# Performance work log

Hardware: AMD Instinct MI355X
Metric: run time of the kernel (lower is better)

## Reference

```python
import jax, jax.numpy as jnp
import numpy as np
import math

IN_FEATURES = 1024
OUT_FEATURES = 1024
N_BANK = 8192
N_LAYER = 12
N_EMBD = 1024


def setup_inputs() -> dict:
    key = jax.random.key(0)
    kq, kk, kv = jax.random.split(key, 3)
    q = jax.random.normal(kq, (4, 2048, IN_FEATURES), dtype=jnp.float32)
    k = 0.02 * jax.random.normal(kk, (N_BANK, IN_FEATURES), dtype=jnp.float32)
    v_std = 2.0 / N_LAYER / math.sqrt(N_EMBD)
    v = v_std * jax.random.normal(kv, (N_BANK, OUT_FEATURES), dtype=jnp.float32)
    return {"q": q, "k": k, "v": v}


def reference(q, k, v):
    # scores: [B, T, N]
    scores = jnp.einsum("btd,nd->btn", q, k)
    # row-wise L2 normalization, scaled by sqrt(N), then exact (erf) GELU
    sqrt_n = jnp.sqrt(jnp.asarray(scores.shape[-1], scores.dtype))
    norm = jnp.linalg.norm(scores, axis=-1, keepdims=True)
    gated = jax.nn.gelu(scores / norm * sqrt_n, approximate=False)
    # out: [B, T, out_features]
    return jnp.einsum("btn,no->bto", gated, v)
```

## Files before the change

kernel.cpp:

```cpp
#include <hip/hip_runtime.h>
#include <hip/hip_bf16.h>
#include <math.h>


#define MROWS 8192
#define DIN   1024
#define NBANK 8192
#define DOUT  1024

typedef float  f32x4  __attribute__((ext_vector_type(4)));
typedef __bf16 bf16x8 __attribute__((ext_vector_type(8)));

__device__ __forceinline__ float bf2f(unsigned short u) {
  union { unsigned int i; float f; } x; x.i = ((unsigned int)u) << 16; return x.f;
}
__device__ __forceinline__ unsigned short f2bf(float f) {
  union { float f; unsigned int i; } x; x.f = f;
  unsigned int u = x.i;
  unsigned int r = (u + 0x7fffu + ((u >> 16) & 1u)) >> 16;
  return (unsigned short)r;
}

__global__ void cvt_kernel(const float* __restrict__ src,
                           unsigned short* __restrict__ dst, int n) {
  int i = (blockIdx.x * 256 + threadIdx.x) * 4;
  if (i >= n) return;
  float4 vv = *(const float4*)(src + i);
  ushort4 o;
  o.x = f2bf(vv.x); o.y = f2bf(vv.y); o.z = f2bf(vv.z); o.w = f2bf(vv.w);
  *(ushort4*)(dst + i) = o;
}

__global__ void transpose_cvt_kernel(const float* __restrict__ src,
                                     unsigned short* __restrict__ dst,
                                     int R, int C) {
  __shared__ float tile[32][33];
  int c0 = blockIdx.x * 32, r0 = blockIdx.y * 32;
  for (int i = threadIdx.y; i < 32; i += 8)
    tile[i][threadIdx.x] = src[(size_t)(r0 + i) * C + c0 + threadIdx.x];
  __syncthreads();
  for (int i = threadIdx.y; i < 32; i += 8)
    dst[(size_t)(c0 + i) * R + r0 + threadIdx.x] = f2bf(tile[threadIdx.x][i]);
}

__global__ void zero_f32_kernel(float* __restrict__ p, int n4) {
  int i = blockIdx.x * 256 + threadIdx.x;
  if (i < n4) ((float4*)p)[i] = make_float4(0.f, 0.f, 0.f, 0.f);
}

__global__ __launch_bounds__(256, 2) void gemm1_kernel(
    const unsigned short* __restrict__ A, const unsigned short* __restrict__ B,
    unsigned short* __restrict__ C, float* __restrict__ sumsq) {
  __shared__ unsigned short As[128 * 64];
  __shared__ unsigned short Bs[128 * 64];
  const int K = DIN, ldc = NBANK;

  const int tid  = threadIdx.x;
  const int lane = tid & 63;
  const int wave = tid >> 6;
  const int wm   = (wave >> 1) * 64;
  const int wn   = (wave & 1) * 64;
  const int quad = lane >> 4;
  const int l16  = lane & 15;

  const size_t m0 = (size_t)blockIdx.y * 128;
  const size_t n0 = (size_t)blockIdx.x * 128;

  const int srow = tid >> 3;
  const int scol = (tid & 7) * 8;
  const unsigned short* Ag = A + (m0 + srow) * (size_t)K + scol;
  const unsigned short* Bg = B + (n0 + srow) * (size_t)K + scol;
  unsigned short* AsW = As + tid * 8;
  unsigned short* BsW = Bs + tid * 8;

  const unsigned short* ArP = As + (wm + l16) * 64 + quad * 8;
  const unsigned short* BrP = Bs + (wn + l16) * 64 + quad * 8;

  f32x4 acc[4][4];
#pragma unroll
  for (int i = 0; i < 4; i++)
#pragma unroll
    for (int j = 0; j < 4; j++) {
      f32x4 z = {0.f, 0.f, 0.f, 0.f};
      acc[i][j] = z;
    }

  for (int k0 = 0; k0 < K; k0 += 64) {
#pragma unroll
    for (int i = 0; i < 4; i++) {
      __builtin_amdgcn_global_load_lds(
          (const __attribute__((address_space(1))) unsigned int*)(Ag + (size_t)i * 32 * K + k0),
          (__attribute__((address_space(3))) unsigned int*)(AsW + i * 2048), 16, 0, 0);
      __builtin_amdgcn_global_load_lds(
          (const __attribute__((address_space(1))) unsigned int*)(Bg + (size_t)i * 32 * K + k0),
          (__attribute__((address_space(3))) unsigned int*)(BsW + i * 2048), 16, 0, 0);
    }
    __syncthreads();

#pragma unroll
    for (int kk = 0; kk < 2; kk++) {
      bf16x8 af[4], bfr[4];
#pragma unroll
      for (int i = 0; i < 4; i++) af[i] = *(const bf16x8*)(ArP + i * 16 * 64 + kk * 32);
#pragma unroll
      for (int j = 0; j < 4; j++) bfr[j] = *(const bf16x8*)(BrP + j * 16 * 64 + kk * 32);
#pragma unroll
      for (int i = 0; i < 4; i++)
#pragma unroll
        for (int j = 0; j < 4; j++)
          acc[i][j] = __builtin_amdgcn_mfma_f32_16x16x32_bf16(af[i], bfr[j],
                                                              acc[i][j], 0, 0, 0);
    }
    __syncthreads();
  }

#pragma unroll
  for (int i = 0; i < 4; i++)
#pragma unroll
    for (int r = 0; r < 4; r++) {
      size_t row = m0 + wm + i * 16 + quad * 4 + r;
      float s = 0.f;
#pragma unroll
      for (int j = 0; j < 4; j++) {
        float val = acc[i][j][r];
        s += val * val;
        C[row * (size_t)ldc + n0 + wn + j * 16 + l16] = f2bf(val);
      }
      s += __shfl_xor(s, 1);
      s += __shfl_xor(s, 2);
      s += __shfl_xor(s, 4);
      s += __shfl_xor(s, 8);
      if (l16 == 0) atomicAdd(&sumsq[row], s);
    }
}

__global__ void finalize_scale_kernel(float* __restrict__ s) {
  int i = blockIdx.x * 256 + threadIdx.x;
  if (i < MROWS) s[i] = sqrtf((float)NBANK / s[i]);
}

__global__ void gelu_kernel(unsigned short* __restrict__ S,
                            const float* __restrict__ scale) {
  size_t idx = ((size_t)blockIdx.x * 256 + threadIdx.x) * 8;
  int row = (int)(idx >> 13);
  float sc = scale[row];
  uint4 vv = *(const uint4*)(S + idx);
  unsigned int w[4] = {vv.x, vv.y, vv.z, vv.w};
#pragma unroll
  for (int e = 0; e < 4; e++) {
    float x0 = bf2f((unsigned short)(w[e] & 0xffffu)) * sc;
    float x1 = bf2f((unsigned short)(w[e] >> 16)) * sc;
    float g0 = 0.5f * x0 * (1.0f + erff(x0 * 0.70710678118654752f));
    float g1 = 0.5f * x1 * (1.0f + erff(x1 * 0.70710678118654752f));
    w[e] = (unsigned int)f2bf(g0) | ((unsigned int)f2bf(g1) << 16);
  }
  uint4 o; o.x = w[0]; o.y = w[1]; o.z = w[2]; o.w = w[3];
  *(uint4*)(S + idx) = o;
}

__global__ __launch_bounds__(512, 2) void gemm2_kernel(
    const unsigned short* __restrict__ A,
    const unsigned short* __restrict__ B,
    float* __restrict__ C) {
  __shared__ unsigned short As[128 * 64];
  __shared__ unsigned short Bs[256 * 64];
  const int K = NBANK, ldc = DOUT;

  const int tid  = threadIdx.x;
  const int lane = tid & 63;
  const int wave = tid >> 6;
  const int wm   = (wave >> 2) * 64;
  const int wn   = (wave & 3) * 64;
  const int quad = lane >> 4;
  const int l16  = lane & 15;

  const size_t m0 = (size_t)blockIdx.y * 128;
  const size_t n0 = (size_t)blockIdx.x * 256;
  const int    ks = blockIdx.z * (K / 2);

  const int srow = tid >> 3;
  const int scol = (tid & 7) * 8;
  const unsigned short* Ag = A + (m0 + srow) * (size_t)K + scol + ks;
  const unsigned short* Bg = B + (n0 + srow) * (size_t)K + scol + ks;
  unsigned short* AsW = As + tid * 8;
  unsigned short* BsW = Bs + tid * 8;

  const unsigned short* ArP = As + (wm + l16) * 64 + quad * 8;
  const unsigned short* BrP = Bs + (wn + l16) * 64 + quad * 8;

  f32x4 acc[4][4];
#pragma unroll
  for (int i = 0; i < 4; i++)
#pragma unroll
    for (int j = 0; j < 4; j++) {
      f32x4 z = {0.f, 0.f, 0.f, 0.f};
      acc[i][j] = z;
    }

  for (int k0 = 0; k0 < K / 2; k0 += 64) {
#pragma unroll
    for (int i = 0; i < 2; i++)
      __builtin_amdgcn_global_load_lds(
          (const __attribute__((address_space(1))) unsigned int*)(Ag + (size_t)i * 64 * K + k0),
          (__attribute__((address_space(3))) unsigned int*)(AsW + i * 4096), 16, 0, 0);
#pragma unroll
    for (int i = 0; i < 4; i++)
      __builtin_amdgcn_global_load_lds(
          (const __attribute__((address_space(1))) unsigned int*)(Bg + (size_t)i * 64 * K + k0),
          (__attribute__((address_space(3))) unsigned int*)(BsW + i * 4096), 16, 0, 0);
    __syncthreads();

#pragma unroll
    for (int kk = 0; kk < 2; kk++) {
      bf16x8 af[4], bfr[4];
#pragma unroll
      for (int i = 0; i < 4; i++) af[i] = *(const bf16x8*)(ArP + i * 16 * 64 + kk * 32);
#pragma unroll
      for (int j = 0; j < 4; j++) bfr[j] = *(const bf16x8*)(BrP + j * 16 * 64 + kk * 32);
#pragma unroll
      for (int i = 0; i < 4; i++)
#pragma unroll
        for (int j = 0; j < 4; j++)
          acc[i][j] = __builtin_amdgcn_mfma_f32_16x16x32_bf16(af[i], bfr[j],
                                                              acc[i][j], 0, 0, 0);
    }
    __syncthreads();
  }

#pragma unroll
  for (int i = 0; i < 4; i++)
#pragma unroll
    for (int j = 0; j < 4; j++)
#pragma unroll
      for (int r = 0; r < 4; r++) {
        size_t row = m0 + wm + i * 16 + quad * 4 + r;
        size_t col = n0 + wn + j * 16 + l16;
        atomicAdd(&C[row * (size_t)ldc + col], acc[i][j][r]);
      }
}

extern "C" void kernel_launch(void* const* d_in, const int* in_sizes, int n_in,
                              void* d_out, int out_size, void* d_ws, size_t ws_size,
                              hipStream_t stream) {
  const float* q = (const float*)d_in[0];
  const float* k = (const float*)d_in[1];
  const float* v = (const float*)d_in[2];
  float* out = (float*)d_out;

  char* ws = (char*)d_ws;
  const size_t MB = 1024ull * 1024ull;
  unsigned short* qb     = (unsigned short*)(ws);
  unsigned short* kb     = (unsigned short*)(ws + 16 * MB);
  unsigned short* vbT    = (unsigned short*)(ws + 32 * MB);
  unsigned short* scores = (unsigned short*)(ws + 48 * MB);
  float*          scale  = (float*)(ws + 176 * MB);

  const int nqk = MROWS * DIN;

  zero_f32_kernel<<<(MROWS * DOUT / 4 + 255) / 256, 256, 0, stream>>>(out,
                                                                      MROWS * DOUT / 4);
  zero_f32_kernel<<<(MROWS / 4 + 255) / 256, 256, 0, stream>>>(scale, MROWS / 4);

  cvt_kernel<<<nqk / 1024, 256, 0, stream>>>(q, qb, nqk);
  cvt_kernel<<<nqk / 1024, 256, 0, stream>>>(k, kb, nqk);
  transpose_cvt_kernel<<<dim3(DOUT / 32, NBANK / 32), dim3(32, 8), 0, stream>>>(
      v, vbT, NBANK, DOUT);

  gemm1_kernel<<<dim3(NBANK / 128, MROWS / 128), 256, 0, stream>>>(qb, kb, scores,
                                                                   scale);

  finalize_scale_kernel<<<MROWS / 256, 256, 0, stream>>>(scale);

  gelu_kernel<<<(MROWS * (size_t)NBANK) / (256 * 8), 256, 0, stream>>>(scores, scale);

  gemm2_kernel<<<dim3(DOUT / 256, MROWS / 128, 2), 512, 0, stream>>>(scores, vbT, out);
}
```

Before: 581.1 us.

## Fuse GELU into second GEMM A-tile load and add register-prefetch swizzled LDS

The standalone GELU pass over the 8192x8192 bf16 score matrix is removed. Instead, gemm2 applies the scale and erf-GELU to each A tile in registers before storing it to LDS. Both GEMMs switch from direct global-to-LDS loads to register prefetch of the next tile, overlapped with MFMA work, and use an XOR-swizzled LDS layout to avoid bank conflicts. gemm2 also shrinks from a 128x256 tile with 512 threads to 128x128 with 256 threads. GELU is now recomputed by every column block of gemm2 (8x redundant), which trades the saved memory round trip for extra ALU work and register pressure.

```diff
diff --git a/kernel.cpp b/kernel.cpp
--- a/kernel.cpp
+++ b/kernel.cpp
@@ -67,14 +67,22 @@
   const size_t n0 = (size_t)blockIdx.x * 128;
 
   const int srow = tid >> 3;
-  const int scol = (tid & 7) * 8;
-  const unsigned short* Ag = A + (m0 + srow) * (size_t)K + scol;
-  const unsigned short* Bg = B + (n0 + srow) * (size_t)K + scol;
-  unsigned short* AsW = As + tid * 8;
-  unsigned short* BsW = Bs + tid * 8;
-
-  const unsigned short* ArP = As + (wm + l16) * 64 + quad * 8;
-  const unsigned short* BrP = Bs + (wn + l16) * 64 + quad * 8;
+  const int sc8  = tid & 7;
+  const unsigned short* Ag = A + (m0 + srow) * (size_t)K + sc8 * 8;
+  const unsigned short* Bg = B + (n0 + srow) * (size_t)K + sc8 * 8;
+  int wOff[4];
+#pragma unroll
+  for (int i = 0; i < 4; i++)
+    wOff[i] = (srow + i * 32) * 64 + ((sc8 ^ (srow & 7)) * 8);
+
+  int rowA[4], rowB[4];
+#pragma unroll
+  for (int i = 0; i < 4; i++) {
+    rowA[i] = (wm + i * 16 + l16) * 64;
+    rowB[i] = (wn + i * 16 + l16) * 64;
+  }
+  const int xo0 = ((quad + 0) ^ (l16 & 7)) * 8;
+  const int xo1 = ((quad + 4) ^ (l16 & 7)) * 8;
 
   f32x4 acc[4][4];
 #pragma unroll
@@ -85,25 +93,38 @@
       acc[i][j] = z;
     }
 
+  uint4 ar[4], br[4];
+#pragma unroll
+  for (int i = 0; i < 4; i++) {
+    ar[i] = *(const uint4*)(Ag + (size_t)i * 32 * K);
+    br[i] = *(const uint4*)(Bg + (size_t)i * 32 * K);
+  }
+
   for (int k0 = 0; k0 < K; k0 += 64) {
+    __syncthreads();
 #pragma unroll
     for (int i = 0; i < 4; i++) {
-      __builtin_amdgcn_global_load_lds(
-          (const __attribute__((address_space(1))) unsigned int*)(Ag + (size_t)i * 32 * K + k0),
-          (__attribute__((address_space(3))) unsigned int*)(AsW + i * 2048), 16, 0, 0);
-      __builtin_amdgcn_global_load_lds(
-          (const __attribute__((address_space(1))) unsigned int*)(Bg + (size_t)i * 32 * K + k0),
-          (__attribute__((address_space(3))) unsigned int*)(BsW + i * 2048), 16, 0, 0);
+      *(uint4*)(As + wOff[i]) = ar[i];
+      *(uint4*)(Bs + wOff[i]) = br[i];
     }
     __syncthreads();
 
+    if (k0 + 64 < K) {
+#pragma unroll
+      for (int i = 0; i < 4; i++) {
+        ar[i] = *(const uint4*)(Ag + (size_t)i * 32 * K + k0 + 64);
+        br[i] = *(const uint4*)(Bg + (size_t)i * 32 * K + k0 + 64);
+      }
+    }
+
 #pragma unroll
     for (int kk = 0; kk < 2; kk++) {
+      const int xo = kk ? xo1 : xo0;
       bf16x8 af[4], bfr[4];
 #pragma unroll
-      for (int i = 0; i < 4; i++) af[i] = *(const bf16x8*)(ArP + i * 16 * 64 + kk * 32);
-#pragma unroll
-      for (int j = 0; j < 4; j++) bfr[j] = *(const bf16x8*)(BrP + j * 16 * 64 + kk * 32);
+      for (int i = 0; i < 4; i++) af[i] = *(const bf16x8*)(As + rowA[i] + xo);
+#pragma unroll
+      for (int j = 0; j < 4; j++) bfr[j] = *(const bf16x8*)(Bs + rowB[j] + xo);
 #pragma unroll
       for (int i = 0; i < 4; i++)
 #pragma unroll
@@ -111,7 +132,6 @@
           acc[i][j] = __builtin_amdgcn_mfma_f32_16x16x32_bf16(af[i], bfr[j],
                                                               acc[i][j], 0, 0, 0);
     }
-    __syncthreads();
   }
 
 #pragma unroll
@@ -139,54 +159,48 @@
   if (i < MROWS) s[i] = sqrtf((float)NBANK / s[i]);
 }
 
-__global__ void gelu_kernel(unsigned short* __restrict__ S,
-                            const float* __restrict__ scale) {
-  size_t idx = ((size_t)blockIdx.x * 256 + threadIdx.x) * 8;
-  int row = (int)(idx >> 13);
-  float sc = scale[row];
-  uint4 vv = *(const uint4*)(S + idx);
-  unsigned int w[4] = {vv.x, vv.y, vv.z, vv.w};
-#pragma unroll
-  for (int e = 0; e < 4; e++) {
-    float x0 = bf2f((unsigned short)(w[e] & 0xffffu)) * sc;
-    float x1 = bf2f((unsigned short)(w[e] >> 16)) * sc;
-    float g0 = 0.5f * x0 * (1.0f + erff(x0 * 0.70710678118654752f));
-    float g1 = 0.5f * x1 * (1.0f + erff(x1 * 0.70710678118654752f));
-    w[e] = (unsigned int)f2bf(g0) | ((unsigned int)f2bf(g1) << 16);
-  }
-  uint4 o; o.x = w[0]; o.y = w[1]; o.z = w[2]; o.w = w[3];
-  *(uint4*)(S + idx) = o;
-}
-
-__global__ __launch_bounds__(512, 2) void gemm2_kernel(
+__global__ __launch_bounds__(256, 2) void gemm2_kernel(
     const unsigned short* __restrict__ A,
     const unsigned short* __restrict__ B,
+    const float* __restrict__ scale,
     float* __restrict__ C) {
   __shared__ unsigned short As[128 * 64];
-  __shared__ unsigned short Bs[256 * 64];
+  __shared__ unsigned short Bs[128 * 64];
   const int K = NBANK, ldc = DOUT;
 
   const int tid  = threadIdx.x;
   const int lane = tid & 63;
   const int wave = tid >> 6;
-  const int wm   = (wave >> 2) * 64;
-  const int wn   = (wave & 3) * 64;
+  const int wm   = (wave >> 1) * 64;
+  const int wn   = (wave & 1) * 64;
   const int quad = lane >> 4;
   const int l16  = lane & 15;
 
   const size_t m0 = (size_t)blockIdx.y * 128;
-  const size_t n0 = (size_t)blockIdx.x * 256;
+  const size_t n0 = (size_t)blockIdx.x * 128;
   const int    ks = blockIdx.z * (K / 2);
 
   const int srow = tid >> 3;
-  const int scol = (tid & 7) * 8;
-  const unsigned short* Ag = A + (m0 + srow) * (size_t)K + scol + ks;
-  const unsigned short* Bg = B + (n0 + srow) * (size_t)K + scol + ks;
-  unsigned short* AsW = As + tid * 8;
-  unsigned short* BsW = Bs + tid * 8;
-
-  const unsigned short* ArP = As + (wm + l16) * 64 + quad * 8;
-  const unsigned short* BrP = Bs + (wn + l16) * 64 + quad * 8;
+  const int sc8  = tid & 7;
+  const unsigned short* Ag = A + (m0 + srow) * (size_t)K + sc8 * 8 + ks;
+  const unsigned short* Bg = B + (n0 + srow) * (size_t)K + sc8 * 8 + ks;
+  int wOff[4];
+#pragma unroll
+  for (int i = 0; i < 4; i++)
+    wOff[i] = (srow + i * 32) * 64 + ((sc8 ^ (srow & 7)) * 8);
+
+  float scA[4];
+#pragma unroll
+  for (int i = 0; i < 4; i++) scA[i] = scale[m0 + srow + i * 32];
+
+  int rowA[4], rowB[4];
+#pragma unroll
+  for (int i = 0; i < 4; i++) {
+    rowA[i] = (wm + i * 16 + l16) * 64;
+    rowB[i] = (wn + i * 16 + l16) * 64;
+  }
+  const int xo0 = ((quad + 0) ^ (l16 & 7)) * 8;
+  const int xo1 = ((quad + 4) ^ (l16 & 7)) * 8;
 
   f32x4 acc[4][4];
 #pragma unroll
@@ -197,26 +211,55 @@
       acc[i][j] = z;
     }
 
+  auto gelu_pack = [](uint4 g, float sc) -> uint4 {
+    unsigned int w[4] = {g.x, g.y, g.z, g.w};
+#pragma unroll
+    for (int e = 0; e < 4; e++) {
+      float x0 = bf2f((unsigned short)(w[e] & 0xffffu)) * sc;
+      float x1 = bf2f((unsigned short)(w[e] >> 16)) * sc;
+      float g0 = 0.5f * x0 * (1.0f + erff(x0 * 0.70710678118654752f));
+      float g1 = 0.5f * x1 * (1.0f + erff(x1 * 0.70710678118654752f));
+      w[e] = (unsigned int)f2bf(g0) | ((unsigned int)f2bf(g1) << 16);
+    }
+    uint4 o; o.x = w[0]; o.y = w[1]; o.z = w[2]; o.w = w[3];
+    return o;
+  };
+
+  uint4 ra[4], rb[4], wa[4];
+#pragma unroll
+  for (int i = 0; i < 4; i++) {
+    ra[i] = *(const uint4*)(Ag + (size_t)i * 32 * K);
+    rb[i] = *(const uint4*)(Bg + (size_t)i * 32 * K);
+  }
+#pragma unroll
+  for (int i = 0; i < 4; i++) wa[i] = gelu_pack(ra[i], scA[i]);
+
   for (int k0 = 0; k0 < K / 2; k0 += 64) {
-#pragma unroll
-    for (int i = 0; i < 2; i++)
-      __builtin_amdgcn_global_load_lds(
-          (const __attribute__((address_space(1))) unsigned int*)(Ag + (size_t)i * 64 * K + k0),
-          (__attribute__((address_space(3))) unsigned int*)(AsW + i * 4096), 16, 0, 0);
-#pragma unroll
-    for (int i = 0; i < 4; i++)
-      __builtin_amdgcn_global_load_lds(
-          (const __attribute__((address_space(1))) unsigned int*)(Bg + (size_t)i * 64 * K + k0),
-          (__attribute__((address_space(3))) unsigned int*)(BsW + i * 4096), 16, 0, 0);
     __syncthreads();
+#pragma unroll
+    for (int i = 0; i < 4; i++) {
+      *(uint4*)(As + wOff[i]) = wa[i];
+      *(uint4*)(Bs + wOff[i]) = rb[i];
+    }
+    __syncthreads();
+
+    const bool more = (k0 + 64 < K / 2);
+    if (more) {
+#pragma unroll
+      for (int i = 0; i < 4; i++) {
+        ra[i] = *(const uint4*)(Ag + (size_t)i * 32 * K + k0 + 64);
+        rb[i] = *(const uint4*)(Bg + (size_t)i * 32 * K + k0 + 64);
+      }
+    }
 
 #pragma unroll
     for (int kk = 0; kk < 2; kk++) {
+      const int xo = kk ? xo1 : xo0;
       bf16x8 af[4], bfr[4];
 #pragma unroll
-      for (int i = 0; i < 4; i++) af[i] = *(const bf16x8*)(ArP + i * 16 * 64 + kk * 32);
-#pragma unroll
-      for (int j = 0; j < 4; j++) bfr[j] = *(const bf16x8*)(BrP + j * 16 * 64 + kk * 32);
+      for (int i = 0; i < 4; i++) af[i] = *(const bf16x8*)(As + rowA[i] + xo);
+#pragma unroll
+      for (int j = 0; j < 4; j++) bfr[j] = *(const bf16x8*)(Bs + rowB[j] + xo);
 #pragma unroll
       for (int i = 0; i < 4; i++)
 #pragma unroll
@@ -224,7 +267,11 @@
           acc[i][j] = __builtin_amdgcn_mfma_f32_16x16x32_bf16(af[i], bfr[j],
                                                               acc[i][j], 0, 0, 0);
     }
-    __syncthreads();
+
+    if (more) {
+#pragma unroll
+      for (int i = 0; i < 4; i++) wa[i] = gelu_pack(ra[i], scA[i]);
+    }
   }
 
 #pragma unroll
@@ -271,7 +318,6 @@
 
   finalize_scale_kernel<<<MROWS / 256, 256, 0, stream>>>(scale);
 
-  gelu_kernel<<<(MROWS * (size_t)NBANK) / (256 * 8), 256, 0, stream>>>(scores, scale);
-
-  gemm2_kernel<<<dim3(DOUT / 256, MROWS / 128, 2), 512, 0, stream>>>(scores, vbT, out);
-}
+  gemm2_kernel<<<dim3(DOUT / 128, MROWS / 128, 2), 256, 0, stream>>>(scores, vbT,
+                                                                     scale, out);
+}
```

Measured after the change: 1.727 ms. 2.97x slower.
